# Kernel tuning notes

Hardware: AMD Instinct MI355X
Metric: run time of the kernel (lower is better)

## Reference

```python
import jax, jax.numpy as jnp
import numpy as np

B, S, D, H, E, K, F, FS = 4, 2048, 1024, 16, 8, 2, 4096, 2048
HD = D // H
EPS = 1e-5
T = B * S
CAP = int(1.25 * K * T / E)  # capacity factor 1.25 -> 2560 tokens/expert


def _ln(x, g, b):
    mu = jnp.mean(x, -1, keepdims=True)
    var = jnp.var(x, -1, keepdims=True)
    return (x - mu) * jax.lax.rsqrt(var + EPS) * g + b


def _forward(x, attention_mask, ln1_g, ln1_b, wq, bq, wk, bk, wv, bv, wo, bo,
             ln2_g, ln2_b, w_router, w1, b1, w2, b2, ws1, bs1, ws2, bs2):
    # ---- pre-LN self-attention + residual ----
    xn = _ln(x, ln1_g, ln1_b)
    q = (xn @ wq + bq).reshape(B, S, H, HD)
    k = (xn @ wk + bk).reshape(B, S, H, HD)
    v = (xn @ wv + bv).reshape(B, S, H, HD)
    scores = jnp.einsum('bqhd,bkhd->bhqk', q, k) / np.float32(np.sqrt(HD))
    scores = jnp.where(attention_mask[:, None, None, :], jnp.finfo(scores.dtype).min, scores)
    p = jax.nn.softmax(scores, axis=-1)
    attn = jnp.einsum('bhqk,bkhd->bqhd', p, v).reshape(B, S, D) @ wo + bo
    x = x + attn
    # ---- pre-LN sparse MoE FFN + residual ----
    xn = _ln(x, ln2_g, ln2_b).reshape(T, D)
    logits = xn.astype(jnp.float32) @ w_router              # router in fp32, [T,E]
    probs = jax.nn.softmax(logits, axis=-1)
    topv, topi = jax.lax.top_k(probs, K)                    # [T,K]
    topv = topv / jnp.sum(topv, -1, keepdims=True)          # renormalize top-k gates
    oh = jax.nn.one_hot(topi, E, dtype=jnp.float32)         # [T,K,E]
    flat = oh.transpose(1, 0, 2).reshape(K * T, E)          # slot-major routing priority
    pos_tok = jnp.sum((jnp.cumsum(flat, axis=0) - 1.0) * flat, -1)  # slot position within expert
    keep = pos_tok < CAP                                    # drop tokens over capacity
    posc = jnp.clip(pos_tok, 0, CAP - 1).astype(jnp.int32)
    eidx = topi.T.reshape(K * T)
    w = topv.T.reshape(K * T) * keep
    xt = jnp.tile(xn, (K, 1)) * keep[:, None]               # [K*T, D]
    disp = jnp.zeros((E, CAP, D), xn.dtype).at[eidx, posc].add(xt)   # dispatch [E,C,D]
    h = jax.nn.gelu(jnp.einsum('ecd,edf->ecf', disp, w1) + b1[:, None, :], approximate=False)
    eo = jnp.einsum('ecf,efd->ecd', h, w2) + b2[:, None, :]          # expert out [E,C,D]
    y = jnp.sum(eo[eidx, posc].reshape(K, T, D) * w.reshape(K, T, 1), axis=0)  # combine
    # shared expert (dense, always active)
    y = y + jax.nn.gelu(xn @ ws1 + bs1, approximate=False) @ ws2 + bs2
    return x + y.reshape(B, S, D)


def setup_inputs() -> dict:
    key = jax.random.key(0)
    ks = jax.random.split(key, 16)
    g = lambda k, shape, fan: jax.random.normal(k, shape, jnp.float32) * (fan ** -0.5)
    return {
        'x': jax.random.normal(ks[0], (B, S, D), jnp.float32),
        'attention_mask': jnp.zeros((B, S), bool),
        'ln1_g': jnp.ones((D,), jnp.float32), 'ln1_b': jnp.zeros((D,), jnp.float32),
        'wq': g(ks[1], (D, D), D), 'bq': jnp.zeros((D,), jnp.float32),
        'wk': g(ks[2], (D, D), D), 'bk': jnp.zeros((D,), jnp.float32),
        'wv': g(ks[3], (D, D), D), 'bv': jnp.zeros((D,), jnp.float32),
        'wo': g(ks[4], (D, D), D), 'bo': jnp.zeros((D,), jnp.float32),
        'ln2_g': jnp.ones((D,), jnp.float32), 'ln2_b': jnp.zeros((D,), jnp.float32),
        'w_router': g(ks[5], (D, E), D),
        'w1': g(ks[6], (E, D, F), D), 'b1': jnp.zeros((E, F), jnp.float32),
        'w2': g(ks[7], (E, F, D), F), 'b2': jnp.zeros((E, D), jnp.float32),
        'ws1': g(ks[8], (D, FS), D), 'bs1': jnp.zeros((FS,), jnp.float32),
        'ws2': g(ks[9], (FS, D), FS), 'bs2': jnp.zeros((D,), jnp.float32),
    }


def reference(x, attention_mask, ln1_g, ln1_b, wq, bq, wk, bk, wv, bv, wo, bo,
              ln2_g, ln2_b, w_router, w1, b1, w2, b2, ws1, bs1, ws2, bs2):
    return _forward(x, attention_mask, ln1_g, ln1_b, wq, bq, wk, bk, wv, bv, wo, bo,
                    ln2_g, ln2_b, w_router, w1, b1, w2, b2, ws1, bs1, ws2, bs2)
```

## Files before the change

### kernel.cpp

```cpp
#include <hip/hip_runtime.h>
#include <hip/hip_bf16.h>
#include <stdint.h>

#define D_ 1024
#define S_ 2048
#define B_ 4
#define H_ 16
#define T_ 8192
#define E_ 8
#define CAP_ 2560
#define F_ 4096
#define FS_ 2048

typedef __attribute__((ext_vector_type(8))) short s8v;
typedef __attribute__((ext_vector_type(4))) float f4v;

#define GLL(gp, lp) __builtin_amdgcn_global_load_lds( \
    (const __attribute__((address_space(1))) unsigned int*)(gp), \
    (__attribute__((address_space(3))) unsigned int*)(lp), 16, 0, 0)

__device__ inline short f2bf(float f) {
    union { float f; unsigned u; } v; v.f = f;
    unsigned r = (v.u + 0x7fffu + ((v.u >> 16) & 1u)) >> 16;
    return (short)(r & 0xffffu);
}
__device__ inline float b2f(short h) {
    union { unsigned u; float f; } v; v.u = ((unsigned)(unsigned short)h) << 16; return v.f;
}
__device__ inline float gelu_f(float x) {
    return 0.5f * x * (1.0f + erff(x * 0.7071067811865475f));
}
__device__ inline f4v f4zero() { f4v z; z[0]=0.f; z[1]=0.f; z[2]=0.f; z[3]=0.f; return z; }

__global__ __launch_bounds__(256) void transcvt(const float* __restrict__ in,
                                                short* __restrict__ out, int R, int C)
{
    __shared__ float tile[32][33];
    const int tid = threadIdx.x;
    const int tx = tid & 31, ty = tid >> 5;
    const long long ib = (long long)blockIdx.z * R * C;
    const int r0 = blockIdx.y * 32, c0 = blockIdx.x * 32;
#pragma unroll
    for (int i = 0; i < 4; i++)
        tile[ty + i * 8][tx] = in[ib + (long long)(r0 + ty + i * 8) * C + c0 + tx];
    __syncthreads();
#pragma unroll
    for (int i = 0; i < 4; i++)
        out[ib + (long long)(c0 + ty + i * 8) * R + r0 + tx] = f2bf(tile[tx][ty + i * 8]);
}

__global__ __launch_bounds__(256) void transcvt2(const float* __restrict__ in,
    short* __restrict__ oh, short* __restrict__ ol, int R, int C)
{
    __shared__ float tile[32][33];
    const int tid = threadIdx.x;
    const int tx = tid & 31, ty = tid >> 5;
    const int r0 = blockIdx.y * 32, c0 = blockIdx.x * 32;
#pragma unroll
    for (int i = 0; i < 4; i++)
        tile[ty + i * 8][tx] = in[(long long)(r0 + ty + i * 8) * C + c0 + tx];
    __syncthreads();
#pragma unroll
    for (int i = 0; i < 4; i++) {
        const float v = tile[tx][ty + i * 8];
        const short h = f2bf(v);
        const long long o = (long long)(c0 + ty + i * 8) * R + r0 + tx;
        oh[o] = h;
        ol[o] = f2bf(v - b2f(h));
    }
}

__global__ __launch_bounds__(256) void ln1_split(const float* __restrict__ x,
    const float* __restrict__ g, const float* __restrict__ bta,
    short* __restrict__ xh, short* __restrict__ xl)
{
    const int t = blockIdx.x, tid = threadIdx.x;
    const float4 v = ((const float4*)(x + (long long)t * D_))[tid];
    float s1 = v.x + v.y + v.z + v.w;
    float s2 = v.x * v.x + v.y * v.y + v.z * v.z + v.w * v.w;
#pragma unroll
    for (int off = 32; off; off >>= 1) { s1 += __shfl_xor(s1, off, 64); s2 += __shfl_xor(s2, off, 64); }
    __shared__ float r1[4], r2[4];
    if ((tid & 63) == 0) { r1[tid >> 6] = s1; r2[tid >> 6] = s2; }
    __syncthreads();
    s1 = r1[0] + r1[1] + r1[2] + r1[3];
    s2 = r2[0] + r2[1] + r2[2] + r2[3];
    const float mu = s1 * (1.0f / D_);
    const float var = s2 * (1.0f / D_) - mu * mu;
    const float rs = rsqrtf(var + 1e-5f);
    const float4 gv = ((const float4*)g)[tid];
    const float4 bv = ((const float4*)bta)[tid];
    float xn[4];
    xn[0] = (v.x - mu) * rs * gv.x + bv.x;
    xn[1] = (v.y - mu) * rs * gv.y + bv.y;
    xn[2] = (v.z - mu) * rs * gv.z + bv.z;
    xn[3] = (v.w - mu) * rs * gv.w + bv.w;
    short4 hh, ll;
    hh.x = f2bf(xn[0]); ll.x = f2bf(xn[0] - b2f(hh.x));
    hh.y = f2bf(xn[1]); ll.y = f2bf(xn[1] - b2f(hh.y));
    hh.z = f2bf(xn[2]); ll.z = f2bf(xn[2] - b2f(hh.z));
    hh.w = f2bf(xn[3]); ll.w = f2bf(xn[3] - b2f(hh.w));
    ((short4*)(xh + (long long)t * D_))[tid] = hh;
    ((short4*)(xl + (long long)t * D_))[tid] = ll;
}

__global__ __launch_bounds__(256) void ln2_router_kernel(const float* __restrict__ x,
    const float* __restrict__ g, const float* __restrict__ bta, const float* __restrict__ wr,
    short* __restrict__ xo, int* __restrict__ topi, float* __restrict__ gates)
{
    const int t = blockIdx.x, tid = threadIdx.x;
    const float4 v = ((const float4*)(x + (long long)t * D_))[tid];
    float s1 = v.x + v.y + v.z + v.w;
    float s2 = v.x * v.x + v.y * v.y + v.z * v.z + v.w * v.w;
#pragma unroll
    for (int off = 32; off; off >>= 1) { s1 += __shfl_xor(s1, off, 64); s2 += __shfl_xor(s2, off, 64); }
    __shared__ float r1[4], r2[4];
    if ((tid & 63) == 0) { r1[tid >> 6] = s1; r2[tid >> 6] = s2; }
    __syncthreads();
    s1 = r1[0] + r1[1] + r1[2] + r1[3];
    s2 = r2[0] + r2[1] + r2[2] + r2[3];
    const float mu = s1 * (1.0f / D_);
    const float var = s2 * (1.0f / D_) - mu * mu;
    const float rs = rsqrtf(var + 1e-5f);
    const float4 gv = ((const float4*)g)[tid];
    const float4 bv = ((const float4*)bta)[tid];
    float xn[4];
    xn[0] = (v.x - mu) * rs * gv.x + bv.x;
    xn[1] = (v.y - mu) * rs * gv.y + bv.y;
    xn[2] = (v.z - mu) * rs * gv.z + bv.z;
    xn[3] = (v.w - mu) * rs * gv.w + bv.w;
    short4 o;
    o.x = f2bf(xn[0]); o.y = f2bf(xn[1]); o.z = f2bf(xn[2]); o.w = f2bf(xn[3]);
    ((short4*)(xo + (long long)t * D_))[tid] = o;

    float a8[8] = {0, 0, 0, 0, 0, 0, 0, 0};
#pragma unroll
    for (int q = 0; q < 4; q++) {
        const int d = tid * 4 + q;
        const float4 w0 = ((const float4*)(wr + d * 8))[0];
        const float4 w1 = ((const float4*)(wr + d * 8))[1];
        a8[0] += xn[q] * w0.x; a8[1] += xn[q] * w0.y; a8[2] += xn[q] * w0.z; a8[3] += xn[q] * w0.w;
        a8[4] += xn[q] * w1.x; a8[5] += xn[q] * w1.y; a8[6] += xn[q] * w1.z; a8[7] += xn[q] * w1.w;
    }
    __shared__ float lred[32];
#pragma unroll
    for (int e = 0; e < 8; e++) {
        float vv = a8[e];
#pragma unroll
        for (int off = 32; off; off >>= 1) vv += __shfl_xor(vv, off, 64);
        if ((tid & 63) == 0) lred[(tid >> 6) * 8 + e] = vv;
    }
    __syncthreads();
    if (tid == 0) {
        float lg[8];
#pragma unroll
        for (int e = 0; e < 8; e++) lg[e] = lred[e] + lred[8 + e] + lred[16 + e] + lred[24 + e];
        int e0 = 0;
        for (int e = 1; e < 8; e++) if (lg[e] > lg[e0]) e0 = e;
        int e1 = (e0 == 0) ? 1 : 0;
        for (int e = 0; e < 8; e++) if (e != e0 && lg[e] > lg[e1]) e1 = e;
        const float mx = lg[e0];
        float den = 0.f;
        for (int e = 0; e < 8; e++) den += expf(lg[e] - mx);
        const float p0 = expf(lg[e0] - mx) / den;
        const float p1 = expf(lg[e1] - mx) / den;
        const float inv = 1.0f / (p0 + p1);
        topi[t * 2] = e0; topi[t * 2 + 1] = e1;
        gates[t * 2] = p0 * inv; gates[t * 2 + 1] = p1 * inv;
    }
}

__global__ __launch_bounds__(256) void route_scan(const int* __restrict__ topi,
    const float* __restrict__ gates, int* __restrict__ posc, float* __restrict__ wv)
{
    const int tid = threadIdx.x;
    const int w = tid >> 6, lane = tid & 63;
    __shared__ int wsum[4 * 8];
    int cnt[8] = {0, 0, 0, 0, 0, 0, 0, 0};
    const int base_r = tid * 64;
    for (int i = 0; i < 64; i++) {
        const int r = base_r + i;
        const int k = r >> 13, t = r & (T_ - 1);
        cnt[topi[t * 2 + k]]++;
    }
    int excl[8];
#pragma unroll
    for (int e = 0; e < 8; e++) {
        int x = cnt[e];
#pragma unroll
        for (int off = 1; off < 64; off <<= 1) {
            int y = __shfl_up(x, off, 64);
            if (lane >= off) x += y;
        }
        excl[e] = x - cnt[e];
        if (lane == 63) wsum[w * 8 + e] = x;
    }
    __syncthreads();
    int pos[8];
#pragma unroll
    for (int e = 0; e < 8; e++) {
        int s = 0;
        for (int ww = 0; ww < 4; ww++) if (ww < w) s += wsum[ww * 8 + e];
        pos[e] = s + excl[e];
    }
    for (int i = 0; i < 64; i++) {
        const int r = base_r + i;
        const int k = r >> 13, t = r & (T_ - 1);
        const int e = topi[t * 2 + k];
        const int p = pos[e]++;
        const bool keep = p < CAP_;
        posc[r] = keep ? p : -1;
        wv[r] = keep ? gates[t * 2 + k] : 0.0f;
    }
}

__global__ __launch_bounds__(128) void dispatch_kernel(const short* __restrict__ xn2,
    const int* __restrict__ topi, const int* __restrict__ posc, short* __restrict__ disp)
{
    const int r = blockIdx.x;
    const int p = posc[r];
    if (p < 0) return;
    const int k = r >> 13, t = r & (T_ - 1);
    const int e = topi[t * 2 + k];
    const int tid = threadIdx.x;
    *(s8v*)&disp[((long long)e * CAP_ + p) * D_ + tid * 8] =
        *(const s8v*)&xn2[(long long)t * D_ + tid * 8];
}

__global__ __launch_bounds__(256) void combine_kernel(const float* __restrict__ x1,
    const float* __restrict__ ys, const float* __restrict__ eo,
    const int* __restrict__ topi, const int* __restrict__ posc,
    const float* __restrict__ wv, float* __restrict__ out)
{
    const int t = blockIdx.x, tid = threadIdx.x;
    float4 a = *(const float4*)&x1[(long long)t * D_ + tid * 4];
    const float4 b = *(const float4*)&ys[(long long)t * D_ + tid * 4];
    a.x += b.x; a.y += b.y; a.z += b.z; a.w += b.w;
#pragma unroll
    for (int k = 0; k < 2; k++) {
        const int r = k * T_ + t;
        const int p = posc[r];
        if (p >= 0) {
            const int e = topi[t * 2 + k];
            const float wt = wv[r];
            const float4 c = *(const float4*)&eo[((long long)e * CAP_ + p) * D_ + tid * 4];
            a.x += wt * c.x; a.y += wt * c.y; a.z += wt * c.z; a.w += wt * c.w;
        }
    }
    *(float4*)&out[(long long)t * D_ + tid * 4] = a;
}

template <int EPI>
__global__ __launch_bounds__(256) void gemm_btz(
    const short* __restrict__ A, const short* __restrict__ Bt,
    const float* __restrict__ bias, void* __restrict__ Cout,
    int M, int N, int K, int ldc,
    long long sA, long long sB, long long sBias, long long sC)
{
    __shared__ __align__(16) short lA[128 * 32];
    __shared__ __align__(16) short lB[128 * 32];
    const int z = blockIdx.z;
    A += (long long)z * sA;
    Bt += (long long)z * sB;
    bias += (long long)z * sBias;
    const int tid = threadIdx.x;
    const int wvi = tid >> 6, lane = tid & 63, lid = lane & 15, quad = lane >> 4;
    const int wm = wvi >> 1, wn = wvi & 1;
    const int mBase = blockIdx.y * 128, nBase = blockIdx.x * 128;
    f4v acc[4][4];
#pragma unroll
    for (int i = 0; i < 4; i++)
#pragma unroll
        for (int j = 0; j < 4; j++) acc[i][j] = f4zero();
    const long long aOff0 = (long long)(mBase + (tid >> 2)) * K + (tid & 3) * 8;
    const long long aOff1 = aOff0 + 64LL * K;
    const long long bOff0 = (long long)(nBase + (tid >> 2)) * K + (tid & 3) * 8;
    const long long bOff1 = bOff0 + 64LL * K;
    const int wofs = wvi << 9;
    for (int k0 = 0; k0 < K; k0 += 32) {
        __syncthreads();
        GLL(A + aOff0 + k0, &lA[wofs]);  GLL(A + aOff1 + k0, &lA[2048 + wofs]);
        GLL(Bt + bOff0 + k0, &lB[wofs]); GLL(Bt + bOff1 + k0, &lB[2048 + wofs]);
        __syncthreads();
        s8v af[4], bf[4];
#pragma unroll
        for (int i = 0; i < 4; i++)
            af[i] = *(const s8v*)&lA[(wm * 64 + i * 16 + lid) * 32 + quad * 8];
#pragma unroll
        for (int j = 0; j < 4; j++)
            bf[j] = *(const s8v*)&lB[(wn * 64 + j * 16 + lid) * 32 + quad * 8];
#pragma unroll
        for (int i = 0; i < 4; i++)
#pragma unroll
            for (int j = 0; j < 4; j++)
                acc[i][j] = __builtin_amdgcn_mfma_f32_16x16x32_bf16(af[i], bf[j], acc[i][j], 0, 0, 0);
    }
    const int mW = mBase + wm * 64 + quad * 4;
    const int nW = nBase + wn * 64 + lid;
    short* Cs = (short*)Cout + (long long)z * sC;
    float* Cf = (float*)Cout + (long long)z * sC;
#pragma unroll
    for (int j = 0; j < 4; j++) {
        const int n = nW + j * 16;
        const float bn = bias[n];
#pragma unroll
        for (int i = 0; i < 4; i++) {
            const int m = mW + i * 16;
#pragma unroll
            for (int r = 0; r < 4; r++) {
                float v = acc[i][j][r] + bn;
                if (EPI == 1) { v = gelu_f(v); Cs[(long long)(m + r) * ldc + n] = f2bf(v); }
                else          { Cf[(long long)(m + r) * ldc + n] = v; }
            }
        }
    }
}

template <int EPI>
__global__ __launch_bounds__(256) void gemm_hl(
    const short* __restrict__ Ah, const short* __restrict__ Al,
    const short* __restrict__ Bh, const short* __restrict__ Bl,
    const float* __restrict__ biasQ, const float* __restrict__ biasK,
    const float* __restrict__ biasV, const float* __restrict__ resid,
    short* __restrict__ Ch, short* __restrict__ Cl, float* __restrict__ Cf,
    int M, int N, int K, int ldc)
{
    __shared__ __align__(16) short lAh[4096], lAl[4096], lBh[4096], lBl[4096];
    const int tid = threadIdx.x;
    const int wvi = tid >> 6, lane = tid & 63, lid = lane & 15, quad = lane >> 4;
    const int wm = wvi >> 1, wn = wvi & 1;
    const int mBase = blockIdx.y * 128, nBase = blockIdx.x * 128;
    f4v acc[4][4];
#pragma unroll
    for (int i = 0; i < 4; i++)
#pragma unroll
        for (int j = 0; j < 4; j++) acc[i][j] = f4zero();
    const long long aOff0 = (long long)(mBase + (tid >> 2)) * K + (tid & 3) * 8;
    const long long aOff1 = aOff0 + 64LL * K;
    const long long bOff0 = (long long)(nBase + (tid >> 2)) * K + (tid & 3) * 8;
    const long long bOff1 = bOff0 + 64LL * K;
    const int wofs = wvi << 9;
    for (int k0 = 0; k0 < K; k0 += 32) {
        __syncthreads();
        GLL(Ah + aOff0 + k0, &lAh[wofs]);  GLL(Ah + aOff1 + k0, &lAh[2048 + wofs]);
        GLL(Al + aOff0 + k0, &lAl[wofs]);  GLL(Al + aOff1 + k0, &lAl[2048 + wofs]);
        GLL(Bh + bOff0 + k0, &lBh[wofs]);  GLL(Bh + bOff1 + k0, &lBh[2048 + wofs]);
        GLL(Bl + bOff0 + k0, &lBl[wofs]);  GLL(Bl + bOff1 + k0, &lBl[2048 + wofs]);
        __syncthreads();
        s8v ah[4], al[4], bh[4], bl[4];
#pragma unroll
        for (int i = 0; i < 4; i++) {
            const int ro = (wm * 64 + i * 16 + lid) * 32 + quad * 8;
            ah[i] = *(const s8v*)&lAh[ro];
            al[i] = *(const s8v*)&lAl[ro];
        }
#pragma unroll
        for (int j = 0; j < 4; j++) {
            const int ro = (wn * 64 + j * 16 + lid) * 32 + quad * 8;
            bh[j] = *(const s8v*)&lBh[ro];
            bl[j] = *(const s8v*)&lBl[ro];
        }
#pragma unroll
        for (int i = 0; i < 4; i++)
#pragma unroll
            for (int j = 0; j < 4; j++) {
                acc[i][j] = __builtin_amdgcn_mfma_f32_16x16x32_bf16(ah[i], bh[j], acc[i][j], 0, 0, 0);
                acc[i][j] = __builtin_amdgcn_mfma_f32_16x16x32_bf16(ah[i], bl[j], acc[i][j], 0, 0, 0);
                acc[i][j] = __builtin_amdgcn_mfma_f32_16x16x32_bf16(al[i], bh[j], acc[i][j], 0, 0, 0);
            }
    }
    const int mW = mBase + wm * 64 + quad * 4;
    const int nW = nBase + wn * 64 + lid;
#pragma unroll
    for (int j = 0; j < 4; j++) {
        const int n = nW + j * 16;
        const float* bp = (n < 1024) ? biasQ : ((n < 2048) ? biasK : biasV);
        const float bn = bp[n & 1023];
#pragma unroll
        for (int i = 0; i < 4; i++) {
            const int m = mW + i * 16;
#pragma unroll
            for (int r = 0; r < 4; r++) {
                const float v = acc[i][j][r] + bn;
                const long long o = (long long)(m + r) * ldc + n;
                if (EPI == 0) {
                    const short h = f2bf(v);
                    Ch[o] = h;
                    Cl[o] = f2bf(v - b2f(h));
                } else {
                    Cf[o] = v + resid[o];
                }
            }
        }
    }
}

__global__ __launch_bounds__(256) void flash_attn_hl(const short* __restrict__ qkvh,
    const short* __restrict__ qkvl, const unsigned char* __restrict__ mask,
    short* __restrict__ attnh, short* __restrict__ attnl)
{
    __shared__ __align__(16) short lKh[32 * 72], lKl[32 * 72];
    __shared__ __align__(16) short lVth[64 * 40], lVtl[64 * 40];
    __shared__ __align__(16) short lPh[4 * 16 * 40], lPl[4 * 16 * 40];
    const int tid = threadIdx.x;
    const int w = tid >> 6, lane = tid & 63, lid = lane & 15, quad = lane >> 4;
    const int bh = blockIdx.y;
    const int b = bh >> 4, h = bh & 15;
    const int q0row = blockIdx.x * 64 + w * 16;

    const long long rowQ = (long long)(b * S_ + q0row + lid) * 3072 + h * 64;
    const s8v qh0 = *(const s8v*)&qkvh[rowQ + quad * 8];
    const s8v qh1 = *(const s8v*)&qkvh[rowQ + 32 + quad * 8];
    const s8v ql0 = *(const s8v*)&qkvl[rowQ + quad * 8];
    const s8v ql1 = *(const s8v*)&qkvl[rowQ + 32 + quad * 8];

    float m_run[4], l_run[4];
    f4v o[4];
#pragma unroll
    for (int r = 0; r < 4; r++) { m_run[r] = -1e30f; l_run[r] = 0.0f; }
#pragma unroll
    for (int dt = 0; dt < 4; dt++) o[dt] = f4zero();

    const unsigned char* mrow = mask + b * S_;
    const int srow = tid >> 3, sgrp = tid & 7;

    for (int c0 = 0; c0 < S_; c0 += 32) {
        __syncthreads();
        {
            const long long gk = (long long)(b * S_ + c0 + srow) * 3072 + 1024 + h * 64 + sgrp * 8;
            *(s8v*)&lKh[srow * 72 + sgrp * 8] = *(const s8v*)&qkvh[gk];
            *(s8v*)&lKl[srow * 72 + sgrp * 8] = *(const s8v*)&qkvl[gk];
            const long long gv = (long long)(b * S_ + c0 + srow) * 3072 + 2048 + h * 64 + sgrp * 8;
            const s8v vh = *(const s8v*)&qkvh[gv];
            const s8v vl = *(const s8v*)&qkvl[gv];
            const int vcol = srow ^ ((sgrp & 3) << 3);
#pragma unroll
            for (int jj = 0; jj < 8; jj++) {
                lVth[(sgrp * 8 + jj) * 40 + vcol] = vh[jj];
                lVtl[(sgrp * 8 + jj) * 40 + vcol] = vl[jj];
            }
        }
        __syncthreads();

        f4v s0 = f4zero(), s1 = f4zero();
        {
            const int r0 = lid * 72 + quad * 8;
            const s8v kh0a = *(const s8v*)&lKh[r0];
            const s8v kh0b = *(const s8v*)&lKh[r0 + 32];
            const s8v kl0a = *(const s8v*)&lKl[r0];
            const s8v kl0b = *(const s8v*)&lKl[r0 + 32];
            s0 = __builtin_amdgcn_mfma_f32_16x16x32_bf16(qh0, kh0a, s0, 0, 0, 0);
            s0 = __builtin_amdgcn_mfma_f32_16x16x32_bf16(qh1, kh0b, s0, 0, 0, 0);
            s0 = __builtin_amdgcn_mfma_f32_16x16x32_bf16(qh0, kl0a, s0, 0, 0, 0);
            s0 = __builtin_amdgcn_mfma_f32_16x16x32_bf16(qh1, kl0b, s0, 0, 0, 0);
            s0 = __builtin_amdgcn_mfma_f32_16x16x32_bf16(ql0, kh0a, s0, 0, 0, 0);
            s0 = __builtin_amdgcn_mfma_f32_16x16x32_bf16(ql1, kh0b, s0, 0, 0, 0);
            const int r1i = (16 + lid) * 72 + quad * 8;
            const s8v kh1a = *(const s8v*)&lKh[r1i];
            const s8v kh1b = *(const s8v*)&lKh[r1i + 32];
            const s8v kl1a = *(const s8v*)&lKl[r1i];
            const s8v kl1b = *(const s8v*)&lKl[r1i + 32];
            s1 = __builtin_amdgcn_mfma_f32_16x16x32_bf16(qh0, kh1a, s1, 0, 0, 0);
            s1 = __builtin_amdgcn_mfma_f32_16x16x32_bf16(qh1, kh1b, s1, 0, 0, 0);
            s1 = __builtin_amdgcn_mfma_f32_16x16x32_bf16(qh0, kl1a, s1, 0, 0, 0);
            s1 = __builtin_amdgcn_mfma_f32_16x16x32_bf16(qh1, kl1b, s1, 0, 0, 0);
            s1 = __builtin_amdgcn_mfma_f32_16x16x32_bf16(ql0, kh1a, s1, 0, 0, 0);
            s1 = __builtin_amdgcn_mfma_f32_16x16x32_bf16(ql1, kh1b, s1, 0, 0, 0);
        }
        const bool mk0 = mrow[c0 + lid] != 0;
        const bool mk1 = mrow[c0 + 16 + lid] != 0;
        float p0[4], p1[4];
#pragma unroll
        for (int r = 0; r < 4; r++) {
            p0[r] = mk0 ? -1e30f : s0[r] * 0.125f;
            p1[r] = mk1 ? -1e30f : s1[r] * 0.125f;
        }
        float mc[4];
#pragma unroll
        for (int r = 0; r < 4; r++) mc[r] = fmaxf(p0[r], p1[r]);
#pragma unroll
        for (int off = 1; off < 16; off <<= 1)
#pragma unroll
            for (int r = 0; r < 4; r++) mc[r] = fmaxf(mc[r], __shfl_xor(mc[r], off, 64));
        float alpha[4], rsum[4];
#pragma unroll
        for (int r = 0; r < 4; r++) {
            const float mn = fmaxf(m_run[r], mc[r]);
            alpha[r] = __expf(m_run[r] - mn);
            m_run[r] = mn;
            p0[r] = __expf(p0[r] - mn);
            p1[r] = __expf(p1[r] - mn);
            rsum[r] = p0[r] + p1[r];
        }
#pragma unroll
        for (int off = 1; off < 16; off <<= 1)
#pragma unroll
            for (int r = 0; r < 4; r++) rsum[r] += __shfl_xor(rsum[r], off, 64);
#pragma unroll
        for (int r = 0; r < 4; r++) l_run[r] = l_run[r] * alpha[r] + rsum[r];
#pragma unroll
        for (int dt = 0; dt < 4; dt++)
#pragma unroll
            for (int r = 0; r < 4; r++) o[dt][r] *= alpha[r];
#pragma unroll
        for (int r = 0; r < 4; r++) {
            const int o0 = w * 640 + (quad * 4 + r) * 40 + lid;
            const short h0 = f2bf(p0[r]);
            const short h1 = f2bf(p1[r]);
            lPh[o0] = h0;      lPl[o0] = f2bf(p0[r] - b2f(h0));
            lPh[o0 + 16] = h1; lPl[o0 + 16] = f2bf(p1[r] - b2f(h1));
        }
        __syncthreads();
        const s8v pah = *(const s8v*)&lPh[w * 640 + lid * 40 + quad * 8];
        const s8v pal = *(const s8v*)&lPl[w * 640 + lid * 40 + quad * 8];
#pragma unroll
        for (int dt = 0; dt < 4; dt++) {
            const int d = dt * 16 + lid;
            const int x3 = (dt * 2 + (lid >> 3)) & 3;
            const int ro = d * 40 + ((quad ^ x3) << 3);
            const s8v bvh = *(const s8v*)&lVth[ro];
            const s8v bvl = *(const s8v*)&lVtl[ro];
            o[dt] = __builtin_amdgcn_mfma_f32_16x16x32_bf16(pah, bvh, o[dt], 0, 0, 0);
            o[dt] = __builtin_amdgcn_mfma_f32_16x16x32_bf16(pah, bvl, o[dt], 0, 0, 0);
            o[dt] = __builtin_amdgcn_mfma_f32_16x16x32_bf16(pal, bvh, o[dt], 0, 0, 0);
        }
    }
#pragma unroll
    for (int dt = 0; dt < 4; dt++)
#pragma unroll
        for (int r = 0; r < 4; r++) {
            const int m = q0row + quad * 4 + r;
            const float v = o[dt][r] / l_run[r];
            const long long idx = (long long)(b * S_ + m) * D_ + h * 64 + dt * 16 + lid;
            const short hh = f2bf(v);
            attnh[idx] = hh;
            attnl[idx] = f2bf(v - b2f(hh));
        }
}

constexpr long long SZ_DD2   = (long long)D_ * D_ * 2;
constexpr long long OFF_WQKVH = 0;
constexpr long long OFF_WQKVL = OFF_WQKVH + 3 * SZ_DD2;
constexpr long long OFF_WOH   = OFF_WQKVL + 3 * SZ_DD2;
constexpr long long OFF_WOL   = OFF_WOH + SZ_DD2;
constexpr long long OFF_W1T   = OFF_WOL + SZ_DD2;
constexpr long long OFF_W2T   = OFF_W1T + (long long)E_ * F_ * D_ * 2;
constexpr long long OFF_WS1T  = OFF_W2T + (long long)E_ * D_ * F_ * 2;
constexpr long long OFF_WS2T  = OFF_WS1T + (long long)FS_ * D_ * 2;
constexpr long long OFF_X1    = OFF_WS2T + (long long)D_ * FS_ * 2;
constexpr long long OFF_XN2   = OFF_X1 + (long long)T_ * D_ * 4;
constexpr long long OFF_TOPI  = OFF_XN2 + (long long)T_ * D_ * 2;
constexpr long long OFF_GATES = OFF_TOPI + (long long)T_ * 2 * 4;
constexpr long long OFF_POSC  = OFF_GATES + (long long)T_ * 2 * 4;
constexpr long long OFF_WVAL  = OFF_POSC + (long long)2 * T_ * 4;
constexpr long long ZONE      = OFF_WVAL + (long long)2 * T_ * 4;
constexpr long long OFF_XH1   = ZONE;
constexpr long long OFF_XL1   = OFF_XH1 + (long long)T_ * D_ * 2;
constexpr long long OFF_QKVH  = OFF_XL1 + (long long)T_ * D_ * 2;
constexpr long long OFF_QKVL  = OFF_QKVH + (long long)T_ * 3 * D_ * 2;
constexpr long long OFF_ATTNH = OFF_QKVL + (long long)T_ * 3 * D_ * 2;
constexpr long long OFF_ATTNL = OFF_ATTNH + (long long)T_ * D_ * 2;
constexpr long long OFF_DISP  = ZONE;
constexpr long long OFF_H     = OFF_DISP + (long long)E_ * CAP_ * D_ * 2;
constexpr long long OFF_EO    = OFF_H + (long long)4 * CAP_ * F_ * 2;
constexpr long long OFF_YS    = OFF_EO + (long long)E_ * CAP_ * D_ * 4;
constexpr long long OFF_HS    = ZONE;

extern "C" void kernel_launch(void* const* d_in, const int* in_sizes, int n_in,
                              void* d_out, int out_size, void* d_ws, size_t ws_size,
                              hipStream_t stream)
{
    (void)in_sizes; (void)n_in; (void)out_size; (void)ws_size;
    const float* x       = (const float*)d_in[0];
    const unsigned char* mask = (const unsigned char*)d_in[1];
    const float* ln1g    = (const float*)d_in[2];
    const float* ln1b    = (const float*)d_in[3];
    const float* wq      = (const float*)d_in[4];
    const float* bq      = (const float*)d_in[5];
    const float* wk      = (const float*)d_in[6];
    const float* bk      = (const float*)d_in[7];
    const float* wvp     = (const float*)d_in[8];
    const float* bvv     = (const float*)d_in[9];
    const float* wo      = (const float*)d_in[10];
    const float* bo      = (const float*)d_in[11];
    const float* ln2g    = (const float*)d_in[12];
    const float* ln2b    = (const float*)d_in[13];
    const float* wrouter = (const float*)d_in[14];
    const float* w1      = (const float*)d_in[15];
    const float* b1      = (const float*)d_in[16];
    const float* w2      = (const float*)d_in[17];
    const float* b2      = (const float*)d_in[18];
    const float* ws1     = (const float*)d_in[19];
    const float* bs1     = (const float*)d_in[20];
    const float* ws2     = (const float*)d_in[21];
    const float* bs2     = (const float*)d_in[22];
    float* out = (float*)d_out;
    char* ws = (char*)d_ws;

    short* wqkvh = (short*)(ws + OFF_WQKVH);
    short* wqkvl = (short*)(ws + OFF_WQKVL);
    short* woh   = (short*)(ws + OFF_WOH);
    short* wol   = (short*)(ws + OFF_WOL);
    short* w1T   = (short*)(ws + OFF_W1T);
    short* w2T   = (short*)(ws + OFF_W2T);
    short* ws1T  = (short*)(ws + OFF_WS1T);
    short* ws2T  = (short*)(ws + OFF_WS2T);
    float* x1    = (float*)(ws + OFF_X1);
    short* xn2   = (short*)(ws + OFF_XN2);
    int*   topi  = (int*)(ws + OFF_TOPI);
    float* gates = (float*)(ws + OFF_GATES);
    int*   posc  = (int*)(ws + OFF_POSC);
    float* wval  = (float*)(ws + OFF_WVAL);
    short* xh1   = (short*)(ws + OFF_XH1);
    short* xl1   = (short*)(ws + OFF_XL1);
    short* qkvh  = (short*)(ws + OFF_QKVH);
    short* qkvl  = (short*)(ws + OFF_QKVL);
    short* attnh = (short*)(ws + OFF_ATTNH);
    short* attnl = (short*)(ws + OFF_ATTNL);
    short* disp  = (short*)(ws + OFF_DISP);
    short* hbuf  = (short*)(ws + OFF_H);
    float* eo    = (float*)(ws + OFF_EO);
    short* hs    = (short*)(ws + OFF_HS);
    float* ysb   = (float*)(ws + OFF_YS);

    const dim3 tb(256);
    transcvt2<<<dim3(32, 32), tb, 0, stream>>>(wq,  wqkvh,               wqkvl,               1024, 1024);
    transcvt2<<<dim3(32, 32), tb, 0, stream>>>(wk,  wqkvh + 1024 * 1024, wqkvl + 1024 * 1024, 1024, 1024);
    transcvt2<<<dim3(32, 32), tb, 0, stream>>>(wvp, wqkvh + 2 * 1024 * 1024, wqkvl + 2 * 1024 * 1024, 1024, 1024);
    transcvt2<<<dim3(32, 32), tb, 0, stream>>>(wo,  woh, wol, 1024, 1024);
    transcvt<<<dim3(128, 32, 8), tb, 0, stream>>>(w1, w1T, 1024, 4096);
    transcvt<<<dim3(32, 128, 8), tb, 0, stream>>>(w2, w2T, 4096, 1024);
    transcvt<<<dim3(64, 32, 1), tb, 0, stream>>>(ws1, ws1T, 1024, 2048);
    transcvt<<<dim3(32, 64, 1), tb, 0, stream>>>(ws2, ws2T, 2048, 1024);

    ln1_split<<<T_, 256, 0, stream>>>(x, ln1g, ln1b, xh1, xl1);

    gemm_hl<0><<<dim3(24, 64), 256, 0, stream>>>(xh1, xl1, wqkvh, wqkvl,
        bq, bk, bvv, nullptr, qkvh, qkvl, nullptr, T_, 3072, 1024, 3072);

    flash_attn_hl<<<dim3(32, 64), 256, 0, stream>>>(qkvh, qkvl, mask, attnh, attnl);

    gemm_hl<1><<<dim3(8, 64), 256, 0, stream>>>(attnh, attnl, woh, wol,
        bo, bo, bo, x, nullptr, nullptr, x1, T_, 1024, 1024, 1024);

    ln2_router_kernel<<<T_, 256, 0, stream>>>(x1, ln2g, ln2b, wrouter, xn2, topi, gates);
    route_scan<<<1, 256, 0, stream>>>(topi, gates, posc, wval);
    dispatch_kernel<<<2 * T_, 128, 0, stream>>>(xn2, topi, posc, disp);

    for (int g = 0; g < 2; g++) {
        const long long e0 = (long long)g * 4;
        gemm_btz<1><<<dim3(32, 20, 4), 256, 0, stream>>>(
            disp + e0 * CAP_ * D_, w1T + e0 * F_ * D_, b1 + e0 * F_, hbuf,
            CAP_, F_, 1024, F_,
            (long long)CAP_ * D_, (long long)F_ * D_, (long long)F_, (long long)CAP_ * F_);
        gemm_btz<2><<<dim3(8, 20, 4), 256, 0, stream>>>(
            hbuf, w2T + e0 * D_ * F_, b2 + e0 * D_, eo + e0 * CAP_ * D_,
            CAP_, 1024, F_, 1024,
            (long long)CAP_ * F_, (long long)D_ * F_, (long long)D_, (long long)CAP_ * D_);
    }

    gemm_btz<1><<<dim3(16, 64, 1), 256, 0, stream>>>(xn2, ws1T, bs1, hs,
        T_, FS_, 1024, FS_, 0, 0, 0, 0);
    gemm_btz<2><<<dim3(8, 64, 1), 256, 0, stream>>>(hs, ws2T, bs2, ysb,
        T_, 1024, FS_, 1024, 0, 0, 0, 0);

    combine_kernel<<<T_, 256, 0, stream>>>(x1, ysb, eo, topi, posc, wval, out);
}
```

Baseline: 2.021 ms.

## Transpose attention MFMA operands so P stays in registers, drop LDS round trip

The flash-attention kernel swaps the A/B operands of the QK^T and PV MFMAs, so each lane holds scores for a single query row. The row max and sum then need only two cross-lane shuffles instead of four-step reductions over four rows. The P tile is packed to bf16 hi/lo pairs and moved into the PV operand layout with register shuffles, which removes the LDS P buffer and one __syncthreads per key chunk. The output is written as vectorised short4 stores, and the mask is read as packed bytes. In exchange there are more ds_bpermute shuffles per chunk, and the operand-layout mapping must be exactly right for the result to stay correct.

```diff
diff --git a/kernel.cpp b/kernel.cpp
--- a/kernel.cpp
+++ b/kernel.cpp
@@ -31,6 +31,13 @@
     return 0.5f * x * (1.0f + erff(x * 0.7071067811865475f));
 }
 __device__ inline f4v f4zero() { f4v z; z[0]=0.f; z[1]=0.f; z[2]=0.f; z[3]=0.f; return z; }
+
+__device__ inline unsigned pk2(float a, float b, unsigned* lo) {
+    const short ha = f2bf(a), hb = f2bf(b);
+    const short la = f2bf(a - b2f(ha)), lb = f2bf(b - b2f(hb));
+    *lo = ((unsigned)(unsigned short)lb << 16) | (unsigned)(unsigned short)la;
+    return ((unsigned)(unsigned short)hb << 16) | (unsigned)(unsigned short)ha;
+}
 
 __global__ __launch_bounds__(256) void transcvt(const float* __restrict__ in,
                                                 short* __restrict__ out, int R, int C)
@@ -401,9 +408,9 @@
 {
     __shared__ __align__(16) short lKh[32 * 72], lKl[32 * 72];
     __shared__ __align__(16) short lVth[64 * 40], lVtl[64 * 40];
-    __shared__ __align__(16) short lPh[4 * 16 * 40], lPl[4 * 16 * 40];
     const int tid = threadIdx.x;
-    const int w = tid >> 6, lane = tid & 63, lid = lane & 15, quad = lane >> 4;
+    const int lane = tid & 63, lid = lane & 15, quad = lane >> 4;
+    const int w = tid >> 6;
     const int bh = blockIdx.y;
     const int b = bh >> 4, h = bh & 15;
     const int q0row = blockIdx.x * 64 + w * 16;
@@ -414,15 +421,15 @@
     const s8v ql0 = *(const s8v*)&qkvl[rowQ + quad * 8];
     const s8v ql1 = *(const s8v*)&qkvl[rowQ + 32 + quad * 8];
 
-    float m_run[4], l_run[4];
+    float m_run = -1e30f, l_run = 0.0f;
     f4v o[4];
-#pragma unroll
-    for (int r = 0; r < 4; r++) { m_run[r] = -1e30f; l_run[r] = 0.0f; }
 #pragma unroll
     for (int dt = 0; dt < 4; dt++) o[dt] = f4zero();
 
     const unsigned char* mrow = mask + b * S_;
     const int srow = tid >> 3, sgrp = tid & 7;
+    const int srcA = lid + ((quad & 1) << 5);
+    const int srcB = srcA + 16;
 
     for (int c0 = 0; c0 < S_; c0 += 32) {
         __syncthreads();
@@ -449,70 +456,75 @@
             const s8v kh0b = *(const s8v*)&lKh[r0 + 32];
             const s8v kl0a = *(const s8v*)&lKl[r0];
             const s8v kl0b = *(const s8v*)&lKl[r0 + 32];
-            s0 = __builtin_amdgcn_mfma_f32_16x16x32_bf16(qh0, kh0a, s0, 0, 0, 0);
-            s0 = __builtin_amdgcn_mfma_f32_16x16x32_bf16(qh1, kh0b, s0, 0, 0, 0);
-            s0 = __builtin_amdgcn_mfma_f32_16x16x32_bf16(qh0, kl0a, s0, 0, 0, 0);
-            s0 = __builtin_amdgcn_mfma_f32_16x16x32_bf16(qh1, kl0b, s0, 0, 0, 0);
-            s0 = __builtin_amdgcn_mfma_f32_16x16x32_bf16(ql0, kh0a, s0, 0, 0, 0);
-            s0 = __builtin_amdgcn_mfma_f32_16x16x32_bf16(ql1, kh0b, s0, 0, 0, 0);
+            s0 = __builtin_amdgcn_mfma_f32_16x16x32_bf16(kh0a, qh0, s0, 0, 0, 0);
+            s0 = __builtin_amdgcn_mfma_f32_16x16x32_bf16(kh0b, qh1, s0, 0, 0, 0);
+            s0 = __builtin_amdgcn_mfma_f32_16x16x32_bf16(kl0a, qh0, s0, 0, 0, 0);
+            s0 = __builtin_amdgcn_mfma_f32_16x16x32_bf16(kl0b, qh1, s0, 0, 0, 0);
+            s0 = __builtin_amdgcn_mfma_f32_16x16x32_bf16(kh0a, ql0, s0, 0, 0, 0);
+            s0 = __builtin_amdgcn_mfma_f32_16x16x32_bf16(kh0b, ql1, s0, 0, 0, 0);
             const int r1i = (16 + lid) * 72 + quad * 8;
             const s8v kh1a = *(const s8v*)&lKh[r1i];
             const s8v kh1b = *(const s8v*)&lKh[r1i + 32];
             const s8v kl1a = *(const s8v*)&lKl[r1i];
             const s8v kl1b = *(const s8v*)&lKl[r1i + 32];
-            s1 = __builtin_amdgcn_mfma_f32_16x16x32_bf16(qh0, kh1a, s1, 0, 0, 0);
-            s1 = __builtin_amdgcn_mfma_f32_16x16x32_bf16(qh1, kh1b, s1, 0, 0, 0);
-            s1 = __builtin_amdgcn_mfma_f32_16x16x32_bf16(qh0, kl1a, s1, 0, 0, 0);
-            s1 = __builtin_amdgcn_mfma_f32_16x16x32_bf16(qh1, kl1b, s1, 0, 0, 0);
-            s1 = __builtin_amdgcn_mfma_f32_16x16x32_bf16(ql0, kh1a, s1, 0, 0, 0);
-            s1 = __builtin_amdgcn_mfma_f32_16x16x32_bf16(ql1, kh1b, s1, 0, 0, 0);
-        }
-        const bool mk0 = mrow[c0 + lid] != 0;
-        const bool mk1 = mrow[c0 + 16 + lid] != 0;
-        float p0[4], p1[4];
+            s1 = __builtin_amdgcn_mfma_f32_16x16x32_bf16(kh1a, qh0, s1, 0, 0, 0);
+            s1 = __builtin_amdgcn_mfma_f32_16x16x32_bf16(kh1b, qh1, s1, 0, 0, 0);
+            s1 = __builtin_amdgcn_mfma_f32_16x16x32_bf16(kl1a, qh0, s1, 0, 0, 0);
+            s1 = __builtin_amdgcn_mfma_f32_16x16x32_bf16(kl1b, qh1, s1, 0, 0, 0);
+            s1 = __builtin_amdgcn_mfma_f32_16x16x32_bf16(kh1a, ql0, s1, 0, 0, 0);
+            s1 = __builtin_amdgcn_mfma_f32_16x16x32_bf16(kh1b, ql1, s1, 0, 0, 0);
+        }
+        const unsigned mm0 = *(const unsigned*)(mrow + c0 + quad * 4);
+        const unsigned mm1 = *(const unsigned*)(mrow + c0 + 16 + quad * 4);
+        float p[8];
 #pragma unroll
         for (int r = 0; r < 4; r++) {
-            p0[r] = mk0 ? -1e30f : s0[r] * 0.125f;
-            p1[r] = mk1 ? -1e30f : s1[r] * 0.125f;
-        }
-        float mc[4];
-#pragma unroll
-        for (int r = 0; r < 4; r++) mc[r] = fmaxf(p0[r], p1[r]);
-#pragma unroll
-        for (int off = 1; off < 16; off <<= 1)
-#pragma unroll
-            for (int r = 0; r < 4; r++) mc[r] = fmaxf(mc[r], __shfl_xor(mc[r], off, 64));
-        float alpha[4], rsum[4];
-#pragma unroll
-        for (int r = 0; r < 4; r++) {
-            const float mn = fmaxf(m_run[r], mc[r]);
-            alpha[r] = __expf(m_run[r] - mn);
-            m_run[r] = mn;
-            p0[r] = __expf(p0[r] - mn);
-            p1[r] = __expf(p1[r] - mn);
-            rsum[r] = p0[r] + p1[r];
-        }
-#pragma unroll
-        for (int off = 1; off < 16; off <<= 1)
-#pragma unroll
-            for (int r = 0; r < 4; r++) rsum[r] += __shfl_xor(rsum[r], off, 64);
-#pragma unroll
-        for (int r = 0; r < 4; r++) l_run[r] = l_run[r] * alpha[r] + rsum[r];
+            p[r]     = ((mm0 >> (8 * r)) & 255u) ? -1e30f : s0[r] * 0.125f;
+            p[4 + r] = ((mm1 >> (8 * r)) & 255u) ? -1e30f : s1[r] * 0.125f;
+        }
+        float mx = fmaxf(fmaxf(fmaxf(p[0], p[1]), fmaxf(p[2], p[3])),
+                         fmaxf(fmaxf(p[4], p[5]), fmaxf(p[6], p[7])));
+        mx = fmaxf(mx, __shfl_xor(mx, 16, 64));
+        mx = fmaxf(mx, __shfl_xor(mx, 32, 64));
+        const float mn = fmaxf(m_run, mx);
+        const float alpha = __expf(m_run - mn);
+        m_run = mn;
+        float rs = 0.0f;
+#pragma unroll
+        for (int i = 0; i < 8; i++) { p[i] = __expf(p[i] - mn); rs += p[i]; }
+        rs += __shfl_xor(rs, 16, 64);
+        rs += __shfl_xor(rs, 32, 64);
+        l_run = l_run * alpha + rs;
 #pragma unroll
         for (int dt = 0; dt < 4; dt++)
 #pragma unroll
-            for (int r = 0; r < 4; r++) o[dt][r] *= alpha[r];
-#pragma unroll
-        for (int r = 0; r < 4; r++) {
-            const int o0 = w * 640 + (quad * 4 + r) * 40 + lid;
-            const short h0 = f2bf(p0[r]);
-            const short h1 = f2bf(p1[r]);
-            lPh[o0] = h0;      lPl[o0] = f2bf(p0[r] - b2f(h0));
-            lPh[o0 + 16] = h1; lPl[o0 + 16] = f2bf(p1[r] - b2f(h1));
-        }
-        __syncthreads();
-        const s8v pah = *(const s8v*)&lPh[w * 640 + lid * 40 + quad * 8];
-        const s8v pal = *(const s8v*)&lPl[w * 640 + lid * 40 + quad * 8];
+            for (int r = 0; r < 4; r++) o[dt][r] *= alpha;
+
+        unsigned c0l, c1l, c2l, c3l;
+        const unsigned c0h = pk2(p[0], p[1], &c0l);
+        const unsigned c1h = pk2(p[2], p[3], &c1l);
+        const unsigned c2h = pk2(p[4], p[5], &c2l);
+        const unsigned c3h = pk2(p[6], p[7], &c3l);
+        union { s8v v; unsigned u[4]; } pah, pal;
+        {
+            const unsigned a0 = __shfl((int)c0h, srcA, 64), a2 = __shfl((int)c2h, srcA, 64);
+            const unsigned a1 = __shfl((int)c1h, srcA, 64), a3 = __shfl((int)c3h, srcA, 64);
+            const unsigned b0 = __shfl((int)c0h, srcB, 64), b2 = __shfl((int)c2h, srcB, 64);
+            const unsigned b1 = __shfl((int)c1h, srcB, 64), b3 = __shfl((int)c3h, srcB, 64);
+            const bool lo = (quad < 2);
+            pah.u[0] = lo ? a0 : a2; pah.u[1] = lo ? a1 : a3;
+            pah.u[2] = lo ? b0 : b2; pah.u[3] = lo ? b1 : b3;
+        }
+        {
+            const unsigned a0 = __shfl((int)c0l, srcA, 64), a2 = __shfl((int)c2l, srcA, 64);
+            const unsigned a1 = __shfl((int)c1l, srcA, 64), a3 = __shfl((int)c3l, srcA, 64);
+            const unsigned b0 = __shfl((int)c0l, srcB, 64), b2 = __shfl((int)c2l, srcB, 64);
+            const unsigned b1 = __shfl((int)c1l, srcB, 64), b3 = __shfl((int)c3l, srcB, 64);
+            const bool lo = (quad < 2);
+            pal.u[0] = lo ? a0 : a2; pal.u[1] = lo ? a1 : a3;
+            pal.u[2] = lo ? b0 : b2; pal.u[3] = lo ? b1 : b3;
+        }
+
 #pragma unroll
         for (int dt = 0; dt < 4; dt++) {
             const int d = dt * 16 + lid;
@@ -520,22 +532,25 @@
             const int ro = d * 40 + ((quad ^ x3) << 3);
             const s8v bvh = *(const s8v*)&lVth[ro];
             const s8v bvl = *(const s8v*)&lVtl[ro];
-            o[dt] = __builtin_amdgcn_mfma_f32_16x16x32_bf16(pah, bvh, o[dt], 0, 0, 0);
-            o[dt] = __builtin_amdgcn_mfma_f32_16x16x32_bf16(pah, bvl, o[dt], 0, 0, 0);
-            o[dt] = __builtin_amdgcn_mfma_f32_16x16x32_bf16(pal, bvh, o[dt], 0, 0, 0);
-        }
-    }
-#pragma unroll
-    for (int dt = 0; dt < 4; dt++)
-#pragma unroll
-        for (int r = 0; r < 4; r++) {
-            const int m = q0row + quad * 4 + r;
-            const float v = o[dt][r] / l_run[r];
-            const long long idx = (long long)(b * S_ + m) * D_ + h * 64 + dt * 16 + lid;
-            const short hh = f2bf(v);
-            attnh[idx] = hh;
-            attnl[idx] = f2bf(v - b2f(hh));
-        }
+            o[dt] = __builtin_amdgcn_mfma_f32_16x16x32_bf16(bvh, pah.v, o[dt], 0, 0, 0);
+            o[dt] = __builtin_amdgcn_mfma_f32_16x16x32_bf16(bvl, pah.v, o[dt], 0, 0, 0);
+            o[dt] = __builtin_amdgcn_mfma_f32_16x16x32_bf16(bvh, pal.v, o[dt], 0, 0, 0);
+        }
+    }
+    const float inv_l = 1.0f / l_run;
+    const long long obase = (long long)(b * S_ + q0row + lid) * D_ + h * 64 + quad * 4;
+#pragma unroll
+    for (int dt = 0; dt < 4; dt++) {
+        short4 hh4, ll4;
+        float v0 = o[dt][0] * inv_l, v1 = o[dt][1] * inv_l;
+        float v2 = o[dt][2] * inv_l, v3 = o[dt][3] * inv_l;
+        hh4.x = f2bf(v0); ll4.x = f2bf(v0 - b2f(hh4.x));
+        hh4.y = f2bf(v1); ll4.y = f2bf(v1 - b2f(hh4.y));
+        hh4.z = f2bf(v2); ll4.z = f2bf(v2 - b2f(hh4.z));
+        hh4.w = f2bf(v3); ll4.w = f2bf(v3 - b2f(hh4.w));
+        *(short4*)&attnh[obase + dt * 16] = hh4;
+        *(short4*)&attnl[obase + dt * 16] = ll4;
+    }
 }
 
 constexpr long long SZ_DD2   = (long long)D_ * D_ * 2;
```

Measured after the change: 1.928 ms. 1.05x faster.
